# Performance work log

Hardware: AMD Instinct MI355X
Metric: run time of the kernel (lower is better)

## Reference

```python
import jax, jax.numpy as jnp
import numpy as np

CR = 64                      # cond_repeat
DILS = tuple(2 ** i for _ in range(2) for i in range(10))  # 2 blocks x 10 layers
Q_ZERO = 128


def setup_inputs() -> dict:
    key = jax.random.key(0)
    B, C, TE = 8, 64, 8          # batch, cond channels, encoding timesteps
    R, S, Q = 128, 128, 256      # residual, skip, classes
    L = len(DILS)
    ks = jax.random.split(key, 12)
    sc = 0.1
    return {
        "encodings": jax.random.normal(ks[0], (B, C, TE), jnp.float32),
        "first_w": jax.random.normal(ks[1], (R, 1, 2), jnp.float32) * sc,
        "first_b": jnp.zeros((R,), jnp.float32),
        "causal_w": jax.random.normal(ks[2], (L, 2 * R, R, 2), jnp.float32) * sc,
        "causal_b": jnp.zeros((L, 2 * R), jnp.float32),
        "cond_w": jax.random.normal(ks[3], (L, 2 * R, C), jnp.float32) * sc,
        "cond_b": jnp.zeros((L, 2 * R), jnp.float32),
        "res_w": jax.random.normal(ks[4], (L, R, R), jnp.float32) * sc,
        "res_b": jnp.zeros((L, R), jnp.float32),
        "skip_w": jax.random.normal(ks[5], (L, S, R), jnp.float32) * sc,
        "skip_b": jnp.zeros((L, S), jnp.float32),
        "skipc_w": jax.random.normal(ks[6], (S, R), jnp.float32) * sc,
        "skipc_b": jnp.zeros((S,), jnp.float32),
        "fc_w": jax.random.normal(ks[7], (S, S), jnp.float32) * sc,
        "fc_b": jnp.zeros((S,), jnp.float32),
        "condf_w": jax.random.normal(ks[8], (S, C), jnp.float32) * sc,
        "condf_b": jnp.zeros((S,), jnp.float32),
        "logits_w": jax.random.normal(ks[9], (Q, S), jnp.float32) * sc,
        "logits_b": jnp.zeros((Q,), jnp.float32),
    }


def _generate(encodings, first_w, first_b, causal_w, causal_b, cond_w, cond_b,
              res_w, res_b, skip_w, skip_b, skipc_w, skipc_b, fc_w, fc_b,
              condf_w, condf_b, logits_w, logits_b):
    B = encodings.shape[0]
    R = res_w.shape[1]
    T = encodings.shape[2] * CR

    # ring buffers emulate QueuedConv1d (queue length = dilation, zero-initialized)
    buf_first0 = jnp.zeros((B, 1), jnp.float32)
    bufs0 = tuple(jnp.zeros((B, d, R), jnp.float32) for d in DILS)
    sample0 = jnp.full((B,), Q_ZERO, jnp.int32)

    def step(carry, t):
        sample, buf_first, bufs = carry
        x = sample.astype(jnp.float32) / 255.0 - 0.5                      # [B]
        c = jax.lax.dynamic_index_in_dim(encodings, t // CR, axis=2,
                                         keepdims=False)                  # [B,C]
        # first causal conv (1 -> R, kernel 2): tap0 on delayed sample, tap1 on current
        prev0 = buf_first[:, 0]
        buf_first = buf_first.at[:, 0].set(x)
        res = (prev0[:, None] * first_w[None, :, 0, 0]
               + x[:, None] * first_w[None, :, 0, 1] + first_b)           # [B,R]
        skip = res @ skipc_w.T + skipc_b                                  # [B,S]
        new_bufs = []
        for l, d in enumerate(DILS):
            idx = jnp.mod(t, d)
            prev = jax.lax.dynamic_index_in_dim(bufs[l], idx, axis=1, keepdims=False)
            new_bufs.append(jax.lax.dynamic_update_index_in_dim(bufs[l], res, idx, axis=1))
            z = (prev @ causal_w[l, :, :, 0].T + res @ causal_w[l, :, :, 1].T
                 + causal_b[l] + c @ cond_w[l].T + cond_b[l])             # [B,2R]
            gate, out = jnp.split(z, 2, axis=1)
            h = jax.nn.sigmoid(gate) * jnp.tanh(out)                      # [B,R]
            res = res + h @ res_w[l].T + res_b[l]
            skip = skip + h @ skip_w[l].T + skip_b[l]
        s = jax.nn.relu(skip) @ fc_w.T + fc_b + c @ condf_w.T + condf_b
        logits = jax.nn.relu(s) @ logits_w.T + logits_b                   # [B,Q]
        sample = jnp.argmax(logits, axis=1).astype(jnp.int32)             # 'max' sampling
        return (sample, buf_first, tuple(new_bufs)), (sample, logits)

    _, (samples, logits) = jax.lax.scan(step, (sample0, buf_first0, bufs0),
                                        jnp.arange(T))
    return samples, logits  # [T,B] int32, [T,B,Q] float32


def reference(encodings, first_w, first_b, causal_w, causal_b, cond_w, cond_b,
              res_w, res_b, skip_w, skip_b, skipc_w, skipc_b, fc_w, fc_b,
              condf_w, condf_b, logits_w, logits_b):
    return _generate(encodings, first_w, first_b, causal_w, causal_b, cond_w, cond_b,
                     res_w, res_b, skip_w, skip_b, skipc_w, skipc_b, fc_w, fc_b,
                     condf_w, condf_b, logits_w, logits_b)
```

## Files before the change

### kernel.cpp

```cpp
#include <hip/hip_runtime.h>
#include <math.h>

#define BB 8
#define TT 512
#define LL 20
#define NBLK 64
#define NTHR 256

typedef float f4 __attribute__((ext_vector_type(4)));
typedef unsigned long long ull;

__constant__ int c_dil[LL] = {1,2,4,8,16,32,64,128,256,512,
                              1,2,4,8,16,32,64,128,256,512};
__constant__ int c_roff[LL] = {-1,0,4096,12288,28672,61440,126976,258048,520192,1044480,
                               2093056,2095104,2099200,2107392,2123776,2156544,
                               2222080,2353152,2615296,3139584};

constexpr size_t OFF_RING = 0;
constexpr size_t OFF_X    = 4188160;

#define P_WC     0
#define P_F      20480
#define P_WST    30208
#define P_WSKIPC 30720
#define P_WFC    30976
#define P_WLOG   31232
#define P_WF0    31744
#define P_WF1    31872
#define P_FB     32000
#define P_CONDZ  32128
#define P_SFC    32768
#define P_RESB   32784
#define P_SKIPB  32824
#define P_ZB     32864
#define P_LOGB   32944
#define P_SKIPCB 32948
#define P_XCUR   32950
#define P_XPREV  32958
#define P_XNEW   32966
#define P_SZ     32976
#define P_SL     33008
#define P_SKACC  33040
#define P_R2     33056
#define P_CF     33072
#define P_PREVF  33600
#define P_HF     34656
#define P_RESF   35712
#define P_RES0   36768
#define POOL_FL  38880

__device__ __forceinline__ f4 ldx(const f4* p) {
    f4 r;
    asm volatile("global_load_dwordx4 %0, %1, off sc0 sc1\n\ts_waitcnt vmcnt(0)"
                 : "=v"(r) : "v"(p) : "memory");
    return r;
}
__device__ __forceinline__ void ldx2(const f4* p0, const f4* p1, f4& a, f4& b) {
    asm volatile("global_load_dwordx4 %0, %2, off sc0 sc1\n\t"
                 "global_load_dwordx4 %1, %3, off sc0 sc1\n\t"
                 "s_waitcnt vmcnt(0)"
                 : "=v"(a), "=v"(b) : "v"(p0), "v"(p1) : "memory");
}
__device__ __forceinline__ void stx(f4* p, f4 v) {
    asm volatile("s_waitcnt vmcnt(0)\n\t"
                 "global_store_dwordx4 %0, %1, off sc0 sc1"
                 :: "v"(p), "v"(v) : "memory");
}

__device__ __forceinline__ void publish16(f4* slot, int J, const float* sl, int e) {
    if (threadIdx.x < 6) {
        int q = threadIdx.x;
        f4 v;
        v.x = sl[3*q];
        v.y = (3*q+1 < 16) ? sl[3*q+1] : 0.f;
        v.z = (3*q+2 < 16) ? sl[3*q+2] : 0.f;
        v.w = __int_as_float(e);
        stx(slot + J*6 + q, v);
    }
}
__device__ __forceinline__ void scat16(float* dst, f4 v, int vi, bool dorelu) {
    int j = vi / 6, q = vi - 6*j;
    #pragma unroll
    for (int i = 0; i < 3; ++i) {
        int E = 3*q + i;
        if (E < 16) {
            float x = v[i];
            if (dorelu) x = fmaxf(x, 0.f);
            dst[(E & 7)*132 + 2*j + (E >> 3)] = x;
        }
    }
}
__device__ __forceinline__ void consume16(const f4* slot, int e, float* dst, bool dorelu) {
    int m = threadIdx.x;
    const f4 *p0 = slot + m, *p1 = slot + 256 + m;
    f4 a, b;
    bool two = (m < 128);
    if (two) ldx2(p0, p1, a, b); else a = ldx(p0);
    while (__float_as_int(a.w) != e) { __builtin_amdgcn_s_sleep(1); a = ldx(p0); }
    if (two) { while (__float_as_int(b.w) != e) { __builtin_amdgcn_s_sleep(1); b = ldx(p1); } }
    scat16(dst, a, m, dorelu);
    if (two) scat16(dst, b, m + 256, dorelu);
}
__device__ __forceinline__ void publish32(f4* slot, int J, const float* sl, int e) {
    if (threadIdx.x < 11) {
        int q = threadIdx.x;
        f4 v;
        v.x = sl[3*q];
        v.y = (3*q+1 < 32) ? sl[3*q+1] : 0.f;
        v.z = (3*q+2 < 32) ? sl[3*q+2] : 0.f;
        v.w = __int_as_float(e);
        stx(slot + J*11 + q, v);
    }
}
__device__ __forceinline__ void scat32(float* dst, f4 v, int vi) {
    int j = vi / 11, q = vi - 11*j;
    #pragma unroll
    for (int i = 0; i < 3; ++i) {
        int E = 3*q + i;
        if (E < 32) dst[(E & 7)*260 + 4*j + (E >> 3)] = v[i];
    }
}
__device__ __forceinline__ void consume32(const f4* slot, int e, float* dst) {
    int m = threadIdx.x;
    const f4 *p0 = slot + m, *p1 = slot + 256 + m, *p2 = slot + 512 + m;
    f4 a, b, c;
    ldx2(p0, p1, a, b);
    bool three = (m < 192);
    if (three) c = ldx(p2);
    while (__float_as_int(a.w) != e) { __builtin_amdgcn_s_sleep(1); a = ldx(p0); }
    while (__float_as_int(b.w) != e) { __builtin_amdgcn_s_sleep(1); b = ldx(p1); }
    if (three) { while (__float_as_int(c.w) != e) { __builtin_amdgcn_s_sleep(1); c = ldx(p2); } }
    scat32(dst, a, m);
    scat32(dst, b, m + 256);
    if (three) scat32(dst, c, m + 512);
}

__global__ __launch_bounds__(NTHR, 1) void wn_gen(
    const float* __restrict__ enc,
    const float* __restrict__ first_w,  const float* __restrict__ first_b,
    const float* __restrict__ causal_w, const float* __restrict__ causal_b,
    const float* __restrict__ cond_w,   const float* __restrict__ cond_b,
    const float* __restrict__ res_w,    const float* __restrict__ res_b,
    const float* __restrict__ skip_w,   const float* __restrict__ skip_b,
    const float* __restrict__ skipc_w,  const float* __restrict__ skipc_b,
    const float* __restrict__ fc_w,     const float* __restrict__ fc_b,
    const float* __restrict__ condf_w,  const float* __restrict__ condf_b,
    const float* __restrict__ logits_w, const float* __restrict__ logits_b,
    float* __restrict__ wsf, float* __restrict__ out)
{
    extern __shared__ float pool[];
    const int tid = threadIdx.x;
    const int J = blockIdx.x;
    float* ring = wsf + OFF_RING;
    f4* xb = (f4*)(wsf + OFF_X);

    for (int m = tid; m < 20480; m += NTHR) {
        int l = m >> 10, rem = m & 1023, g = rem >> 8, i = rem & 255;
        int grow = (g < 2) ? (2*J + g) : (128 + 2*J + (g - 2));
        int col = i & 127, k = i >> 7;
        pool[P_WC + m] = causal_w[((size_t)(l*256 + grow)*128 + col)*2 + k];
    }
    if (tid < 256) {
        int r = tid >> 7, i = tid & 127;
        pool[P_WSKIPC + tid] = skipc_w[(size_t)(2*J + r)*128 + i];
        pool[P_WFC + tid]    = fc_w[(size_t)(2*J + r)*128 + i];
    }
    for (int m = tid; m < 512; m += NTHR) {
        int w = m >> 7, i = m & 127;
        pool[P_WLOG + m] = logits_w[(size_t)(4*J + w)*128 + i];
    }
    if (tid < 128) {
        pool[P_WF0 + tid] = first_w[2*tid];
        pool[P_WF1 + tid] = first_w[2*tid + 1];
        pool[P_FB + tid]  = first_b[tid];
    }
    if (tid < 40) {
        int l = tid >> 1, r = tid & 1;
        pool[P_RESB + tid]  = res_b[l*128 + 2*J + r];
        pool[P_SKIPB + tid] = skip_b[l*128 + 2*J + r];
    }
    if (tid < 4) pool[P_LOGB + tid] = logits_b[4*J + tid];
    if (tid < 2) pool[P_SKIPCB + tid] = skipc_b[2*J + tid];
    for (int m = tid; m < 2112; m += NTHR) pool[P_RES0 + m] = 0.f;
    if (tid < 8) { pool[P_XCUR + tid] = 128.f/255.f - 0.5f; pool[P_XPREV + tid] = 0.f; }
    __syncthreads();

    for (int l = 0; l < 19; ++l) {
        for (int m = tid; m < 512; m += NTHR) {
            int g = m >> 7, j = m & 127;
            const float* w1 = pool + P_WC + ((l+1)*4 + g)*256 + 128;
            const float* rw = res_w + (size_t)l*128*128 + j;
            float acc = 0.f;
            #pragma unroll 8
            for (int i = 0; i < 128; ++i) acc += w1[i] * rw[(size_t)i*128];
            pool[P_F + (l*4 + g)*128 + j] = acc;
        }
    }
    if (tid < 80) {
        int l = tid >> 2, g = tid & 3;
        float acc = 0.f;
        if (l >= 1) {
            const float* w1 = pool + P_WC + (l*4 + g)*256 + 128;
            for (int i = 0; i < 128; ++i) acc += w1[i] * res_b[(l-1)*128 + i];
        }
        pool[P_ZB + tid] = acc;
    }
    __syncthreads();

    int e = 0;
    int er_pending = 0;

    for (int t = 0; t < TT; ++t) {
        if ((t & 63) == 0) {
            int te = t >> 6;
            for (int m = tid; m < 512; m += NTHR) {
                int b = m >> 6, j = m & 63;
                pool[P_CF + b*66 + j] = enc[(size_t)b*512 + j*8 + te];
            }
            __syncthreads();
            for (int m = tid; m < 640; m += NTHR) {
                int l = m >> 5, rem = m & 31, g = rem >> 3, b = rem & 7;
                int grow = (g < 2) ? (2*J + g) : (128 + 2*J + (g - 2));
                float acc = causal_b[l*256 + grow] + cond_b[l*256 + grow]
                          + pool[P_ZB + l*4 + g];
                const float* cw = cond_w + (size_t)(l*256 + grow)*64;
                const float* cf = pool + P_CF + b*66;
                for (int j = 0; j < 64; ++j) acc += cw[j]*cf[j];
                pool[P_CONDZ + l*32 + g*8 + b] = acc;
            }
            if (tid < 16) {
                int r = tid >> 3, b = tid & 7, row = 2*J + r;
                float acc = fc_b[row] + condf_b[row];
                const float* cw = condf_w + (size_t)row*64;
                const float* cf = pool + P_CF + b*66;
                for (int j = 0; j < 64; ++j) acc += cw[j]*cf[j];
                pool[P_SFC + r*8 + b] = acc;
            }
            __syncthreads();
        }

        const int cur = t & 1;
        for (int m = tid; m < 1024; m += NTHR) {
            int b = m >> 7, r = m & 127;
            pool[P_RES0 + cur*1056 + b*132 + r] =
                pool[P_XPREV + b]*pool[P_WF0 + r] + pool[P_XCUR + b]*pool[P_WF1 + r] + pool[P_FB + r];
        }
        __syncthreads();
        {
            int w = tid >> 6, lane = tid & 63, b = lane >> 3, k = lane & 7;
            if (w < 2) {
                const float* wr = pool + P_WSKIPC + w*128;
                const float* rs = pool + P_RES0 + cur*1056 + b*132;
                float acc = 0.f;
                #pragma unroll
                for (int i = 0; i < 16; ++i) { int j = k + 8*i; acc += wr[j]*rs[j]; }
                acc += __shfl_xor(acc,1); acc += __shfl_xor(acc,2); acc += __shfl_xor(acc,4);
                if (k == 0) pool[P_SKACC + w*8 + b] = acc + pool[P_SKIPCB + w];
            }
        }
        if (tid < 16) {
            int r = tid >> 3, b = tid & 7;
            pool[P_R2 + r*8 + b] = pool[P_RES0 + cur*1056 + b*132 + 2*J + r];
        }

        for (int l = 0; l < LL; ++l) {
            {
                int g = tid >> 6, lane = tid & 63, b = lane >> 3, k = lane & 7;
                const float* w0 = pool + P_WC + (l*4 + g)*256;
                const float* pv = ((l == 0) ? pool + P_RES0 + (cur^1)*1056 : pool + P_PREVF) + b*132;
                const float* rs = ((l <= 1) ? pool + P_RES0 + cur*1056 : pool + P_RESF) + b*132;
                float acc = 0.f;
                #pragma unroll
                for (int i = 0; i < 16; ++i) {
                    int j = k + 8*i;
                    acc += w0[j]*pv[j] + w0[128 + j]*rs[j];
                }
                if (l >= 1) {
                    const float* fm = pool + P_F + ((l-1)*4 + g)*128;
                    const float* hh = pool + P_HF + b*132;
                    #pragma unroll
                    for (int i = 0; i < 16; ++i) { int j = k + 8*i; acc += fm[j]*hh[j]; }
                }
                acc += __shfl_xor(acc,1); acc += __shfl_xor(acc,2); acc += __shfl_xor(acc,4);
                if (k == 0) pool[P_SZ + g*8 + b] = acc;
            }
            __syncthreads();
            if (tid < 16) {
                int r = tid & 1, b = tid >> 1;
                float g = pool[P_SZ + r*8 + b]     + pool[P_CONDZ + l*32 + r*8 + b];
                float o = pool[P_SZ + (2+r)*8 + b] + pool[P_CONDZ + l*32 + (2+r)*8 + b];
                pool[P_SL + r*8 + b] = (1.f/(1.f + expf(-g))) * tanhf(o);
            }
            __syncthreads();
            ++e; int eh = e;
            publish16(xb + (size_t)(eh & 3)*768, J, pool + P_SL, eh);
            float wv0, wv1;
            {
                int r0 = tid >> 7, i0 = tid & 127;
                wv0 = res_w [(size_t)(l*128 + 2*J + r0)*128 + i0];
                wv1 = skip_w[(size_t)(l*128 + 2*J + r0)*128 + i0];
            }
            ull pfa = 0, pfb = 0;
            if (l <= 18) {
                int d = c_dil[l+1];
                if (t >= d) {
                    int slot = (t - d) & (2*d - 1);
                    const float* rp = ring + c_roff[l+1] + (size_t)slot*1024 + tid*4;
                    pfa = __hip_atomic_load((const ull*)rp,     __ATOMIC_RELAXED, __HIP_MEMORY_SCOPE_AGENT);
                    pfb = __hip_atomic_load((const ull*)(rp+2), __ATOMIC_RELAXED, __HIP_MEMORY_SCOPE_AGENT);
                }
            }
            if (l >= 1 && l <= 18)
                consume16(xb + (size_t)(er_pending & 3)*768, er_pending, pool + P_RESF, false);
            consume16(xb + (size_t)(eh & 3)*768, eh, pool + P_HF, false);
            pool[P_WST + tid] = wv0;
            pool[P_WST + 256 + tid] = wv1;
            __syncthreads();
            {
                int w = tid >> 6, lane = tid & 63, b = lane >> 3, k = lane & 7;
                int r = w & 1, isSkip = w >> 1;
                if (isSkip || l <= 18) {
                    const float* wr = pool + P_WST + (isSkip ? 256 : 0) + r*128;
                    const float* hh = pool + P_HF + b*132;
                    float acc = 0.f;
                    #pragma unroll
                    for (int i = 0; i < 16; ++i) { int j = k + 8*i; acc += wr[j]*hh[j]; }
                    acc += __shfl_xor(acc,1); acc += __shfl_xor(acc,2); acc += __shfl_xor(acc,4);
                    if (k == 0) {
                        if (isSkip) {
                            pool[P_SKACC + r*8 + b] += acc + pool[P_SKIPB + l*2 + r];
                        } else {
                            float v = pool[P_R2 + r*8 + b] + acc + pool[P_RESB + l*2 + r];
                            pool[P_R2 + r*8 + b] = v;
                            pool[P_SL + r*8 + b] = v;
                            int d = c_dil[l+1];
                            int slot = t & (2*d - 1);
                            float* wp = ring + c_roff[l+1] + (size_t)slot*1024 + b*128 + 2*J + r;
                            __hip_atomic_store(wp, v, __ATOMIC_RELAXED, __HIP_MEMORY_SCOPE_AGENT);
                        }
                    }
                }
            }
            __syncthreads();
            if (l <= 17) {
                ++e;
                publish16(xb + (size_t)(e & 3)*768, J, pool + P_SL, e);
                er_pending = e;
            }
            if (l <= 18) {
                int b = tid >> 5, c = (tid & 31)*4;
                union { ull u; float f[2]; } u0, u1;
                u0.u = pfa; u1.u = pfb;
                float* dp = pool + P_PREVF + b*132 + c;
                dp[0] = u0.f[0]; dp[1] = u0.f[1]; dp[2] = u1.f[0]; dp[3] = u1.f[1];
            }
            __syncthreads();
        }

        ++e;
        publish16(xb + (size_t)(e & 3)*768, J, pool + P_SKACC, e);
        consume16(xb + (size_t)(e & 3)*768, e, pool + P_HF, false);
        __syncthreads();
        {
            int w = tid >> 6, lane = tid & 63, b = lane >> 3, k = lane & 7;
            if (w < 2) {
                const float* wr = pool + P_WFC + w*128;
                const float* sk = pool + P_HF + b*132;
                float acc = 0.f;
                #pragma unroll
                for (int i = 0; i < 16; ++i) { int j = k + 8*i; acc += wr[j]*fmaxf(sk[j], 0.f); }
                acc += __shfl_xor(acc,1); acc += __shfl_xor(acc,2); acc += __shfl_xor(acc,4);
                if (k == 0) pool[P_SL + w*8 + b] = acc + pool[P_SFC + w*8 + b];
            }
        }
        __syncthreads();
        ++e;
        publish16(xb + (size_t)(e & 3)*768, J, pool + P_SL, e);
        consume16(xb + (size_t)(e & 3)*768, e, pool + P_RESF, true);
        __syncthreads();
        {
            int g = tid >> 6, lane = tid & 63, b = lane >> 3, k = lane & 7;
            const float* wr = pool + P_WLOG + g*128;
            const float* sv = pool + P_RESF + b*132;
            float acc = 0.f;
            #pragma unroll
            for (int i = 0; i < 16; ++i) { int j = k + 8*i; acc += wr[j]*sv[j]; }
            acc += __shfl_xor(acc,1); acc += __shfl_xor(acc,2); acc += __shfl_xor(acc,4);
            if (k == 0) {
                float v = acc + pool[P_LOGB + g];
                pool[P_SZ + g*8 + b] = v;
                out[4096 + ((size_t)(t*BB + b))*256 + 4*J + g] = v;
            }
        }
        __syncthreads();
        ++e;
        publish32(xb + (size_t)(e & 3)*768, J, pool + P_SZ, e);
        consume32(xb + (size_t)(e & 3)*768, e, pool + P_PREVF);
        __syncthreads();
        {
            int b = tid >> 5, j = tid & 31;
            float best = -3.4e38f; int bi = 0;
            for (int s = 0; s < 8; ++s) {
                int q = s*32 + j;
                float v = pool[P_PREVF + b*260 + q];
                if (v > best) { best = v; bi = q; }
            }
            for (int m = 16; m >= 1; m >>= 1) {
                float ov = __shfl_xor(best, m, 32);
                int   oi = __shfl_xor(bi, m, 32);
                if (ov > best || (ov == best && oi < bi)) { best = ov; bi = oi; }
            }
            if (j == 0) {
                pool[P_XNEW + b] = (float)bi;
                if (J == 0) out[t*BB + b] = (float)bi;
            }
        }
        __syncthreads();
        if (tid < 8) {
            pool[P_XPREV + tid] = pool[P_XCUR + tid];
            pool[P_XCUR + tid]  = pool[P_XNEW + tid]*(1.f/255.f) - 0.5f;
        }
        __syncthreads();
    }
}

extern "C" void kernel_launch(void* const* d_in, const int* in_sizes, int n_in,
                              void* d_out, int out_size, void* d_ws, size_t ws_size,
                              hipStream_t stream) {
    const float* enc      = (const float*)d_in[0];
    const float* first_w  = (const float*)d_in[1];
    const float* first_b  = (const float*)d_in[2];
    const float* causal_w = (const float*)d_in[3];
    const float* causal_b = (const float*)d_in[4];
    const float* cond_w   = (const float*)d_in[5];
    const float* cond_b   = (const float*)d_in[6];
    const float* res_w    = (const float*)d_in[7];
    const float* res_b    = (const float*)d_in[8];
    const float* skip_w   = (const float*)d_in[9];
    const float* skip_b   = (const float*)d_in[10];
    const float* skipc_w  = (const float*)d_in[11];
    const float* skipc_b  = (const float*)d_in[12];
    const float* fc_w     = (const float*)d_in[13];
    const float* fc_b     = (const float*)d_in[14];
    const float* condf_w  = (const float*)d_in[15];
    const float* condf_b  = (const float*)d_in[16];
    const float* logits_w = (const float*)d_in[17];
    const float* logits_b = (const float*)d_in[18];

    float* wsf = (float*)d_ws;
    float* out = (float*)d_out;

    wn_gen<<<NBLK, NTHR, POOL_FL*4, stream>>>(
        enc, first_w, first_b, causal_w, causal_b, cond_w, cond_b,
        res_w, res_b, skip_w, skip_b, skipc_w, skipc_b, fc_w, fc_b,
        condf_w, condf_b, logits_w, logits_b, wsf, out);
}
```

Measured before the change: 37.41 ms.

## Fold first layer algebraically, merge exchanges, and do local argmax before broadcast

Layer 0's pre-activation and the skip-conv start are now computed in closed form from precomputed weight products and the last three samples. This removes the layer-0 dot products and the residual ring for the first conv. Several cross-block exchanges are merged or pipelined. The residual and h consumes are combined into one batch of loads, the skip publish is issued early from spare waves, and the logits exchange now sends each block's local (max, index) pair instead of all 256 logits. Spin-loop sleeps and the pre-store waitcnt are dropped, and a few __syncthreads are removed. This aims to cut per-step latency, at the cost of more complex sequencing and possible memory-ordering risk.

```diff
diff --git a/kernel.cpp b/kernel.cpp
--- a/kernel.cpp
+++ b/kernel.cpp
@@ -35,19 +35,19 @@
 #define P_ZB     32864
 #define P_LOGB   32944
 #define P_SKIPCB 32948
-#define P_XCUR   32950
-#define P_XPREV  32958
-#define P_XNEW   32966
-#define P_SZ     32976
-#define P_SL     33008
-#define P_SKACC  33040
-#define P_R2     33056
-#define P_CF     33072
-#define P_PREVF  33600
-#define P_HF     34656
-#define P_RESF   35712
-#define P_RES0   36768
-#define POOL_FL  38880
+#define P_Z0C    32952
+#define P_SKC    32976
+#define P_XS     32984
+#define P_SZ     33008
+#define P_SL     33040
+#define P_SKACC  33072
+#define P_R2     33088
+#define P_CF     33104
+#define P_PREVF  33632
+#define P_HF     34688
+#define P_RESF   35744
+#define P_RES0   36800
+#define POOL_FL  37856
 
 __device__ __forceinline__ f4 ldx(const f4* p) {
     f4 r;
@@ -61,33 +61,59 @@
                  "s_waitcnt vmcnt(0)"
                  : "=v"(a), "=v"(b) : "v"(p0), "v"(p1) : "memory");
 }
+__device__ __forceinline__ void ld4x(const f4* a0, const f4* a1, const f4* a2, const f4* a3,
+                                     f4& r0, f4& r1, f4& r2, f4& r3) {
+    asm volatile("global_load_dwordx4 %0, %4, off sc0 sc1\n\t"
+                 "global_load_dwordx4 %1, %5, off sc0 sc1\n\t"
+                 "global_load_dwordx4 %2, %6, off sc0 sc1\n\t"
+                 "global_load_dwordx4 %3, %7, off sc0 sc1\n\t"
+                 "s_waitcnt vmcnt(0)"
+                 : "=v"(r0), "=v"(r1), "=v"(r2), "=v"(r3)
+                 : "v"(a0), "v"(a1), "v"(a2), "v"(a3) : "memory");
+}
 __device__ __forceinline__ void stx(f4* p, f4 v) {
-    asm volatile("s_waitcnt vmcnt(0)\n\t"
-                 "global_store_dwordx4 %0, %1, off sc0 sc1"
+    asm volatile("global_store_dwordx4 %0, %1, off sc0 sc1"
                  :: "v"(p), "v"(v) : "memory");
 }
-
+__device__ __forceinline__ void spin(const f4* p, int e, f4& a) {
+    while (__float_as_int(a.w) != e) a = ldx(p);
+}
+
+__device__ __forceinline__ float pick16(const float* sl, int V) {
+    if (V < 8) return sl[V];
+    if (V >= 9 && V < 17) return sl[V - 1];
+    return 0.f;
+}
 __device__ __forceinline__ void publish16(f4* slot, int J, const float* sl, int e) {
     if (threadIdx.x < 6) {
         int q = threadIdx.x;
         f4 v;
-        v.x = sl[3*q];
-        v.y = (3*q+1 < 16) ? sl[3*q+1] : 0.f;
-        v.z = (3*q+2 < 16) ? sl[3*q+2] : 0.f;
+        v.x = pick16(sl, 3*q);
+        v.y = pick16(sl, 3*q + 1);
+        v.z = pick16(sl, 3*q + 2);
         v.w = __int_as_float(e);
         stx(slot + J*6 + q, v);
     }
+}
+__device__ __forceinline__ void publish_half(f4* slot, int J, int r, const float* half8,
+                                             int e, int m) {
+    int base = 3*m;
+    f4 v;
+    v.x = half8[base];
+    v.y = (base + 1 < 8) ? half8[base + 1] : 0.f;
+    v.z = (base + 2 < 8) ? half8[base + 2] : 0.f;
+    v.w = __int_as_float(e);
+    stx(slot + J*6 + 3*r + m, v);
 }
 __device__ __forceinline__ void scat16(float* dst, f4 v, int vi, bool dorelu) {
     int j = vi / 6, q = vi - 6*j;
     #pragma unroll
     for (int i = 0; i < 3; ++i) {
-        int E = 3*q + i;
-        if (E < 16) {
-            float x = v[i];
-            if (dorelu) x = fmaxf(x, 0.f);
-            dst[(E & 7)*132 + 2*j + (E >> 3)] = x;
-        }
+        int V = 3*q + i;
+        float x = v[i];
+        if (dorelu) x = fmaxf(x, 0.f);
+        if (V < 8)                 dst[V*132 + 2*j]           = x;
+        else if (V >= 9 && V < 17) dst[(V - 9)*132 + 2*j + 1] = x;
     }
 }
 __device__ __forceinline__ void consume16(const f4* slot, int e, float* dst, bool dorelu) {
@@ -96,43 +122,27 @@
     f4 a, b;
     bool two = (m < 128);
     if (two) ldx2(p0, p1, a, b); else a = ldx(p0);
-    while (__float_as_int(a.w) != e) { __builtin_amdgcn_s_sleep(1); a = ldx(p0); }
-    if (two) { while (__float_as_int(b.w) != e) { __builtin_amdgcn_s_sleep(1); b = ldx(p1); } }
+    spin(p0, e, a);
+    if (two) spin(p1, e, b);
     scat16(dst, a, m, dorelu);
     if (two) scat16(dst, b, m + 256, dorelu);
 }
-__device__ __forceinline__ void publish32(f4* slot, int J, const float* sl, int e) {
-    if (threadIdx.x < 11) {
-        int q = threadIdx.x;
-        f4 v;
-        v.x = sl[3*q];
-        v.y = (3*q+1 < 32) ? sl[3*q+1] : 0.f;
-        v.z = (3*q+2 < 32) ? sl[3*q+2] : 0.f;
-        v.w = __int_as_float(e);
-        stx(slot + J*11 + q, v);
-    }
-}
-__device__ __forceinline__ void scat32(float* dst, f4 v, int vi) {
-    int j = vi / 11, q = vi - 11*j;
-    #pragma unroll
-    for (int i = 0; i < 3; ++i) {
-        int E = 3*q + i;
-        if (E < 32) dst[(E & 7)*260 + 4*j + (E >> 3)] = v[i];
-    }
-}
-__device__ __forceinline__ void consume32(const f4* slot, int e, float* dst) {
+__device__ __forceinline__ void consume_pair(const f4* sR, int eR, float* dR,
+                                             const f4* sH, int eH, float* dH) {
     int m = threadIdx.x;
-    const f4 *p0 = slot + m, *p1 = slot + 256 + m, *p2 = slot + 512 + m;
-    f4 a, b, c;
-    ldx2(p0, p1, a, b);
-    bool three = (m < 192);
-    if (three) c = ldx(p2);
-    while (__float_as_int(a.w) != e) { __builtin_amdgcn_s_sleep(1); a = ldx(p0); }
-    while (__float_as_int(b.w) != e) { __builtin_amdgcn_s_sleep(1); b = ldx(p1); }
-    if (three) { while (__float_as_int(c.w) != e) { __builtin_amdgcn_s_sleep(1); c = ldx(p2); } }
-    scat32(dst, a, m);
-    scat32(dst, b, m + 256);
-    if (three) scat32(dst, c, m + 512);
+    const f4 *pra = sR + m, *prb = sR + 256 + m, *pha = sH + m, *phb = sH + 256 + m;
+    f4 ra, rb, ha, hb;
+    bool two = (m < 128);
+    if (two) ld4x(pra, prb, pha, phb, ra, rb, ha, hb);
+    else     ldx2(pra, pha, ra, ha);
+    spin(pra, eR, ra);
+    if (two) spin(prb, eR, rb);
+    scat16(dR, ra, m, false);
+    if (two) scat16(dR, rb, m + 256, false);
+    spin(pha, eH, ha);
+    if (two) spin(phb, eH, hb);
+    scat16(dH, ha, m, false);
+    if (two) scat16(dH, hb, m + 256, false);
 }
 
 __global__ __launch_bounds__(NTHR, 1) void wn_gen(
@@ -181,8 +191,11 @@
     }
     if (tid < 4) pool[P_LOGB + tid] = logits_b[4*J + tid];
     if (tid < 2) pool[P_SKIPCB + tid] = skipc_b[2*J + tid];
-    for (int m = tid; m < 2112; m += NTHR) pool[P_RES0 + m] = 0.f;
-    if (tid < 8) { pool[P_XCUR + tid] = 128.f/255.f - 0.5f; pool[P_XPREV + tid] = 0.f; }
+    if (tid < 8) {
+        pool[P_XS + tid]      = 128.f/255.f - 0.5f;
+        pool[P_XS + 8 + tid]  = 0.f;
+        pool[P_XS + 16 + tid] = 0.f;
+    }
     __syncthreads();
 
     for (int l = 0; l < 19; ++l) {
@@ -205,10 +218,38 @@
         }
         pool[P_ZB + tid] = acc;
     }
+    if (tid < 4) {
+        const float* w0 = pool + P_WC + tid*256;
+        const float* w1 = w0 + 128;
+        float kp = 0.f, kc = 0.f, u = 0.f, c1 = 0.f, a0 = 0.f;
+        for (int j = 0; j < 128; ++j) {
+            float f0 = pool[P_WF0 + j], f1 = pool[P_WF1 + j], fbv = pool[P_FB + j];
+            kp += w0[j]*fbv; kc += w1[j]*fbv;
+            u  += w0[j]*f0;  c1 += w0[j]*f1 + w1[j]*f0;  a0 += w1[j]*f1;
+        }
+        pool[P_Z0C + tid*6 + 0] = kp;
+        pool[P_Z0C + tid*6 + 1] = kc;
+        pool[P_Z0C + tid*6 + 2] = u;
+        pool[P_Z0C + tid*6 + 3] = c1;
+        pool[P_Z0C + tid*6 + 4] = a0;
+    }
+    if (tid < 2) {
+        const float* wr = pool + P_WSKIPC + tid*128;
+        float sk = pool[P_SKIPCB + tid], sa = 0.f, sb = 0.f;
+        for (int j = 0; j < 128; ++j) {
+            sk += wr[j]*pool[P_FB + j];
+            sa += wr[j]*pool[P_WF0 + j];
+            sb += wr[j]*pool[P_WF1 + j];
+        }
+        pool[P_SKC + tid*3 + 0] = sk;
+        pool[P_SKC + tid*3 + 1] = sa;
+        pool[P_SKC + tid*3 + 2] = sb;
+    }
     __syncthreads();
 
     int e = 0;
     int er_pending = 0;
+    int esk = 0;
 
     for (int t = 0; t < TT; ++t) {
         if ((t & 63) == 0) {
@@ -239,61 +280,71 @@
             __syncthreads();
         }
 
-        const int cur = t & 1;
+        ++e; const int eh0 = e;
+        {
+            if (tid < 16) {
+                int r = tid & 1, b = tid >> 1;
+                float kf  = (t >= 1) ? 1.f : 0.f;
+                float x0v = pool[P_XS + b];
+                float x1v = pool[P_XS + 8 + b];
+                float x2v = pool[P_XS + 16 + b];
+                const float* zc = pool + P_Z0C;
+                int g0 = r, g1 = 2 + r;
+                float zg = kf*zc[g0*6+0] + zc[g0*6+1] + x2v*zc[g0*6+2]
+                         + x1v*zc[g0*6+3] + x0v*zc[g0*6+4] + pool[P_CONDZ + g0*8 + b];
+                float zo = kf*zc[g1*6+0] + zc[g1*6+1] + x2v*zc[g1*6+2]
+                         + x1v*zc[g1*6+3] + x0v*zc[g1*6+4] + pool[P_CONDZ + g1*8 + b];
+                pool[P_SL + r*8 + b] = (1.f/(1.f + expf(-zg))) * tanhf(zo);
+            }
+            publish16(xb + (size_t)(eh0 & 3)*768, J, pool + P_SL, eh0);
+        }
         for (int m = tid; m < 1024; m += NTHR) {
             int b = m >> 7, r = m & 127;
-            pool[P_RES0 + cur*1056 + b*132 + r] =
-                pool[P_XPREV + b]*pool[P_WF0 + r] + pool[P_XCUR + b]*pool[P_WF1 + r] + pool[P_FB + r];
-        }
-        __syncthreads();
-        {
-            int w = tid >> 6, lane = tid & 63, b = lane >> 3, k = lane & 7;
-            if (w < 2) {
-                const float* wr = pool + P_WSKIPC + w*128;
-                const float* rs = pool + P_RES0 + cur*1056 + b*132;
-                float acc = 0.f;
-                #pragma unroll
-                for (int i = 0; i < 16; ++i) { int j = k + 8*i; acc += wr[j]*rs[j]; }
-                acc += __shfl_xor(acc,1); acc += __shfl_xor(acc,2); acc += __shfl_xor(acc,4);
-                if (k == 0) pool[P_SKACC + w*8 + b] = acc + pool[P_SKIPCB + w];
-            }
+            pool[P_RES0 + b*132 + r] =
+                pool[P_FB + r] + pool[P_XS + 8 + b]*pool[P_WF0 + r]
+                               + pool[P_XS + b]    *pool[P_WF1 + r];
         }
         if (tid < 16) {
             int r = tid >> 3, b = tid & 7;
-            pool[P_R2 + r*8 + b] = pool[P_RES0 + cur*1056 + b*132 + 2*J + r];
+            float x0v = pool[P_XS + b], x1v = pool[P_XS + 8 + b];
+            pool[P_SKACC + r*8 + b] = pool[P_SKC + r*3] + x1v*pool[P_SKC + r*3 + 1]
+                                                        + x0v*pool[P_SKC + r*3 + 2];
+            int row = 2*J + r;
+            pool[P_R2 + r*8 + b] = pool[P_FB + row] + x1v*pool[P_WF0 + row]
+                                                    + x0v*pool[P_WF1 + row];
         }
 
         for (int l = 0; l < LL; ++l) {
-            {
-                int g = tid >> 6, lane = tid & 63, b = lane >> 3, k = lane & 7;
-                const float* w0 = pool + P_WC + (l*4 + g)*256;
-                const float* pv = ((l == 0) ? pool + P_RES0 + (cur^1)*1056 : pool + P_PREVF) + b*132;
-                const float* rs = ((l <= 1) ? pool + P_RES0 + cur*1056 : pool + P_RESF) + b*132;
-                float acc = 0.f;
-                #pragma unroll
-                for (int i = 0; i < 16; ++i) {
-                    int j = k + 8*i;
-                    acc += w0[j]*pv[j] + w0[128 + j]*rs[j];
-                }
-                if (l >= 1) {
+            int ehh;
+            if (l == 0) {
+                ehh = eh0;
+            } else {
+                {
+                    int g = tid >> 6, lane = tid & 63, b = lane >> 3, k = lane & 7;
+                    const float* w0 = pool + P_WC + (l*4 + g)*256;
+                    const float* pv = pool + P_PREVF + b*132;
+                    const float* rs = ((l == 1) ? pool + P_RES0 : pool + P_RESF) + b*132;
                     const float* fm = pool + P_F + ((l-1)*4 + g)*128;
                     const float* hh = pool + P_HF + b*132;
+                    float acc = 0.f;
                     #pragma unroll
-                    for (int i = 0; i < 16; ++i) { int j = k + 8*i; acc += fm[j]*hh[j]; }
+                    for (int i = 0; i < 16; ++i) {
+                        int j = k + 8*i;
+                        acc += w0[j]*pv[j] + w0[128 + j]*rs[j] + fm[j]*hh[j];
+                    }
+                    acc += __shfl_xor(acc,1); acc += __shfl_xor(acc,2); acc += __shfl_xor(acc,4);
+                    if (k == 0) pool[P_SZ + g*8 + b] = acc;
                 }
-                acc += __shfl_xor(acc,1); acc += __shfl_xor(acc,2); acc += __shfl_xor(acc,4);
-                if (k == 0) pool[P_SZ + g*8 + b] = acc;
-            }
-            __syncthreads();
-            if (tid < 16) {
-                int r = tid & 1, b = tid >> 1;
-                float g = pool[P_SZ + r*8 + b]     + pool[P_CONDZ + l*32 + r*8 + b];
-                float o = pool[P_SZ + (2+r)*8 + b] + pool[P_CONDZ + l*32 + (2+r)*8 + b];
-                pool[P_SL + r*8 + b] = (1.f/(1.f + expf(-g))) * tanhf(o);
-            }
-            __syncthreads();
-            ++e; int eh = e;
-            publish16(xb + (size_t)(eh & 3)*768, J, pool + P_SL, eh);
+                __syncthreads();
+                ++e; ehh = e;
+                if (tid < 16) {
+                    int r = tid & 1, b = tid >> 1;
+                    float g = pool[P_SZ + r*8 + b]     + pool[P_CONDZ + l*32 + r*8 + b];
+                    float o = pool[P_SZ + (2+r)*8 + b] + pool[P_CONDZ + l*32 + (2+r)*8 + b];
+                    pool[P_SL + r*8 + b] = (1.f/(1.f + expf(-g))) * tanhf(o);
+                }
+                publish16(xb + (size_t)(ehh & 3)*768, J, pool + P_SL, ehh);
+            }
             float wv0, wv1;
             {
                 int r0 = tid >> 7, i0 = tid & 127;
@@ -310,9 +361,14 @@
                     pfb = __hip_atomic_load((const ull*)(rp+2), __ATOMIC_RELAXED, __HIP_MEMORY_SCOPE_AGENT);
                 }
             }
-            if (l >= 1 && l <= 18)
-                consume16(xb + (size_t)(er_pending & 3)*768, er_pending, pool + P_RESF, false);
-            consume16(xb + (size_t)(eh & 3)*768, eh, pool + P_HF, false);
+            if (l == 0) {
+                consume16(xb + (size_t)(ehh & 3)*768, ehh, pool + P_HF, false);
+            } else if (l <= 18) {
+                consume_pair(xb + (size_t)(er_pending & 3)*768, er_pending, pool + P_RESF,
+                             xb + (size_t)(ehh & 3)*768,        ehh,        pool + P_HF);
+            } else {
+                consume16(xb + (size_t)(ehh & 3)*768, ehh, pool + P_HF, false);
+            }
             pool[P_WST + tid] = wv0;
             pool[P_WST + 256 + tid] = wv1;
             __syncthreads();
@@ -341,11 +397,19 @@
                     }
                 }
             }
-            __syncthreads();
-            if (l <= 17) {
-                ++e;
-                publish16(xb + (size_t)(e & 3)*768, J, pool + P_SL, e);
-                er_pending = e;
+            {
+                int w = tid >> 6, lane = tid & 63;
+                if (l <= 17) {
+                    ++e; er_pending = e;
+                    if (w < 2 && lane < 3)
+                        publish_half(xb + (size_t)(e & 3)*768, J, w,
+                                     pool + P_SL + w*8, e, lane);
+                } else if (l == 19) {
+                    ++e; esk = e;
+                    if (w >= 2 && lane < 3)
+                        publish_half(xb + (size_t)(e & 3)*768, J, w - 2,
+                                     pool + P_SKACC + (w - 2)*8, e, lane);
+                }
             }
             if (l <= 18) {
                 int b = tid >> 5, c = (tid & 31)*4;
@@ -357,9 +421,7 @@
             __syncthreads();
         }
 
-        ++e;
-        publish16(xb + (size_t)(e & 3)*768, J, pool + P_SKACC, e);
-        consume16(xb + (size_t)(e & 3)*768, e, pool + P_HF, false);
+        consume16(xb + (size_t)(esk & 3)*768, esk, pool + P_HF, false);
         __syncthreads();
         {
             int w = tid >> 6, lane = tid & 63, b = lane >> 3, k = lane & 7;
@@ -373,52 +435,58 @@
                 if (k == 0) pool[P_SL + w*8 + b] = acc + pool[P_SFC + w*8 + b];
             }
         }
-        __syncthreads();
         ++e;
-        publish16(xb + (size_t)(e & 3)*768, J, pool + P_SL, e);
+        {
+            int w = tid >> 6, lane = tid & 63;
+            if (w < 2 && lane < 3)
+                publish_half(xb + (size_t)(e & 3)*768, J, w, pool + P_SL + w*8, e, lane);
+        }
         consume16(xb + (size_t)(e & 3)*768, e, pool + P_RESF, true);
         __syncthreads();
         {
-            int g = tid >> 6, lane = tid & 63, b = lane >> 3, k = lane & 7;
+            int b = tid >> 5, g = (tid >> 3) & 3, k = tid & 7;
             const float* wr = pool + P_WLOG + g*128;
             const float* sv = pool + P_RESF + b*132;
             float acc = 0.f;
             #pragma unroll
             for (int i = 0; i < 16; ++i) { int j = k + 8*i; acc += wr[j]*sv[j]; }
             acc += __shfl_xor(acc,1); acc += __shfl_xor(acc,2); acc += __shfl_xor(acc,4);
-            if (k == 0) {
-                float v = acc + pool[P_LOGB + g];
-                pool[P_SZ + g*8 + b] = v;
-                out[4096 + ((size_t)(t*BB + b))*256 + 4*J + g] = v;
-            }
+            float v = acc + pool[P_LOGB + g];
+            float best = (k == 0) ? v : -3.4e38f;
+            int bi = 4*J + g;
+            { float ov = __shfl_xor(best, 8);  int oi = __shfl_xor(bi, 8);
+              if (ov > best || (ov == best && oi < bi)) { best = ov; bi = oi; } }
+            { float ov = __shfl_xor(best, 16); int oi = __shfl_xor(bi, 16);
+              if (ov > best || (ov == best && oi < bi)) { best = ov; bi = oi; } }
+            if (k == 0) out[4096 + ((size_t)(t*BB + b))*256 + 4*J + g] = v;
+            if ((tid & 31) == 0) { pool[P_SL + b] = best; pool[P_SL + 8 + b] = (float)bi; }
         }
         __syncthreads();
         ++e;
-        publish32(xb + (size_t)(e & 3)*768, J, pool + P_SZ, e);
-        consume32(xb + (size_t)(e & 3)*768, e, pool + P_PREVF);
+        publish16(xb + (size_t)(e & 3)*768, J, pool + P_SL, e);
+        consume16(xb + (size_t)(e & 3)*768, e, pool + P_HF, false);
         __syncthreads();
-        {
-            int b = tid >> 5, j = tid & 31;
-            float best = -3.4e38f; int bi = 0;
-            for (int s = 0; s < 8; ++s) {
-                int q = s*32 + j;
-                float v = pool[P_PREVF + b*260 + q];
-                if (v > best) { best = v; bi = q; }
-            }
-            for (int m = 16; m >= 1; m >>= 1) {
-                float ov = __shfl_xor(best, m, 32);
-                int   oi = __shfl_xor(bi, m, 32);
-                if (ov > best || (ov == best && oi < bi)) { best = ov; bi = oi; }
-            }
-            if (j == 0) {
-                pool[P_XNEW + b] = (float)bi;
-                if (J == 0) out[t*BB + b] = (float)bi;
-            }
-        }
-        __syncthreads();
-        if (tid < 8) {
-            pool[P_XPREV + tid] = pool[P_XCUR + tid];
-            pool[P_XCUR + tid]  = pool[P_XNEW + tid]*(1.f/255.f) - 0.5f;
+        if (tid < 64) {
+            int b = tid >> 3, j0 = tid & 7;
+            float best = -3.4e38f; float bidx = 0.f;
+            #pragma unroll
+            for (int k2 = 0; k2 < 8; ++k2) {
+                int j = j0*8 + k2;
+                float v  = pool[P_HF + b*132 + 2*j];
+                float id = pool[P_HF + b*132 + 2*j + 1];
+                if (v > best || (v == best && id < bidx)) { best = v; bidx = id; }
+            }
+            #pragma unroll
+            for (int m = 4; m >= 1; m >>= 1) {
+                float ov = __shfl_xor(best, m); float oi = __shfl_xor(bidx, m);
+                if (ov > best || (ov == best && oi < bidx)) { best = ov; bidx = oi; }
+            }
+            if (j0 == 0) {
+                if (J == 0) out[t*BB + b] = bidx;
+                pool[P_XS + 16 + b] = pool[P_XS + 8 + b];
+                pool[P_XS + 8 + b]  = pool[P_XS + b];
+                pool[P_XS + b]      = bidx*(1.f/255.f) - 0.5f;
+            }
         }
         __syncthreads();
     }
```

Result: faster. 35.99 ms (-3.8%).
